# Optimization experiments

Hardware: AMD Instinct MI355X
Metric: run time of the kernel (lower is better)

## Reference

```python
import jax, jax.numpy as jnp
import numpy as np
from jax import lax

B, D, S, H, W, T = 128, 512, 30, 14, 14, 12


def setup_inputs() -> dict:
    key = jax.random.key(0)
    ks = jax.random.split(key, 28)
    f = lambda k, shape: jax.random.normal(k, shape, jnp.float32) * 0.05
    return {
        "q": f(ks[0], (B, D)),
        "cws": f(ks[1], (B, D, S)),
        "KB": f(ks[2], (B, D, H, W)),
        "c0": f(ks[3], (B, D)),
        "m0": f(ks[4], (B, D)),
        "Wq": f(ks[5], (D, D)), "bq": f(ks[6], (D,)),
        "Wct": f(ks[7], (2 * D, D)), "bct": f(ks[8], (D,)),
        "wca": f(ks[9], (D,)), "bca": f(ks[10], ()),
        "Wm": f(ks[11], (D, D)), "bm": f(ks[12], (D,)),
        "Wkb": f(ks[13], (D, D)), "bkb": f(ks[14], (D,)),
        "Wrm": f(ks[15], (2 * D, D)), "brm": f(ks[16], (D,)),
        "wra": f(ks[17], (D,)), "bra": f(ks[18], ()),
        "Wwm": f(ks[19], (2 * D, D)), "bwm": f(ks[20], (D,)),
        "wwa": f(ks[21], (D,)), "bwa": f(ks[22], ()),
        "Wam": f(ks[23], (2 * D, D)), "bam": f(ks[24], (D,)),
        "Wg": f(ks[25], (D, D)), "bg": f(ks[26], (D,)),
        "steps": T,
    }


def _mac(q, cws, KB, c0, m0, Wq, bq, Wct, bct, wca, bca, Wm, bm, Wkb, bkb,
         Wrm, brm, wra, bra, Wwm, bwm, wwa, bwa, Wam, bam, Wg, bg, steps):
    b, d, h, w = KB.shape[0], KB.shape[1], KB.shape[2], KB.shape[3]
    KBp = jnp.transpose(KB, (0, 2, 3, 1))          # B,H,W,d
    KB2 = KBp @ Wkb + bkb                           # KB_transform (step-invariant)
    q_i = q @ Wq + bq                               # q_transform (step-invariant)

    nhist = steps + 1
    c_hist = jnp.zeros((nhist, b, d), KB.dtype).at[0].set(c0)
    m_hist = jnp.zeros((nhist, b, d), KB.dtype).at[0].set(m0)

    def step(carry, t):
        c_hist, m_hist, c_prev, m_prev = carry
        # ---- ControlUnit ----
        cq = jnp.concatenate([q_i, c_prev], axis=-1) @ Wct + bct   # B,d
        clog = jnp.einsum('bds,d->bs', cq[:, :, None] * cws, wca) + bca
        cattn = jax.nn.softmax(clog, axis=-1)                       # B,S
        c_i = jnp.einsum('bs,bds->bd', cattn, cws)
        # ---- ReadUnit ----
        mp = m_prev @ Wm + bm                                       # B,d
        I = mp[:, None, None, :] * KB2                              # B,H,W,d
        Im = jnp.concatenate([I, KBp], axis=-1) @ Wrm + brm         # B,H,W,d
        rlog = jnp.einsum('bhwd,d->bhw', c_i[:, None, None, :] * Im, wra) + bra
        rattn = jax.nn.softmax(rlog.reshape(b, -1), axis=-1).reshape(b, h, w)
        m_new = jnp.einsum('bhw,bhwd->bd', rattn, KBp)
        # ---- WriteUnit (self_attn + mem_gate) ----
        _m = jnp.concatenate([m_new, m_prev], axis=-1) @ Wwm + bwm
        slog = jnp.einsum('tbd,d->bt', c_i[None] * c_hist, wwa) + bwa
        valid = jnp.arange(nhist) <= t
        slog = jnp.where(valid[None, :], slog, jnp.float32(-1e9))
        sattn = jax.nn.softmax(slog, axis=-1)                       # B,T+1
        m_sa = jnp.einsum('bt,tbd->bd', sattn, m_hist)
        _m = jnp.concatenate([m_sa, _m], axis=-1) @ Wam + bam
        g = jax.nn.sigmoid(c_i @ Wg + bg)
        _m = g * m_prev + (1.0 - g) * _m
        c_hist = c_hist.at[t + 1].set(c_i)
        m_hist = m_hist.at[t + 1].set(_m)
        return (c_hist, m_hist, c_i, _m), None

    (c_hist, m_hist, c_last, m_last), _ = lax.scan(
        step, (c_hist, m_hist, c0, m0), jnp.arange(steps))
    return m_last


def reference(q, cws, KB, c0, m0, Wq, bq, Wct, bct, wca, bca, Wm, bm, Wkb, bkb,
              Wrm, brm, wra, bra, Wwm, bwm, wwa, bwa, Wam, bam, Wg, bg, steps):
    return _mac(q, cws, KB, c0, m0, Wq, bq, Wct, bct, wca, bca, Wm, bm, Wkb, bkb,
                Wrm, brm, wra, bra, Wwm, bwm, wwa, bwa, Wam, bam, Wg, bg, steps)
```

## Files before the change

kernel.cpp:

```cpp
#include <hip/hip_runtime.h>
#include <cstdint>

#define BB 128
#define DD 512
#define SS 30
#define PP 196
#define TT 12
#define BD (BB*DD)

typedef unsigned short ushortT;
typedef unsigned int uintT;

__device__ __forceinline__ float bf2f(ushortT u)
{
    return __uint_as_float(((uintT)u) << 16);
}
__device__ __forceinline__ ushortT f2bf(float f)
{
    uintT b = __float_as_uint(f);
    return (ushortT)((b + 0x7FFFu + ((b >> 16) & 1u)) >> 16);
}

struct GDesc {
    const float *A0, *A1;
    const ushortT *W0, *W1;
    const float *bias;
    float *out;
    const float *e1;
    int nparts, epi, mblk, nblk, aux;
};
struct GPack { GDesc d[6]; };

__global__ __launch_bounds__(256)
void gemm4(GPack pk)
{
    GDesc d = pk.d[blockIdx.z];
    if ((int)blockIdx.x >= d.mblk || (int)blockIdx.y >= d.nblk) return;
    const int tid  = threadIdx.x;
    const int lane = tid & 63;
    const int wv   = __builtin_amdgcn_readfirstlane(tid >> 6);

    if (d.epi == 5) {
        int bb = (blockIdx.x * 4 + blockIdx.y) * 2;
        #pragma unroll
        for (int b = bb; b < bb + 2; ++b) {
            const float* sat = d.e1 + b * 16;
            float a0 = 0.f, a1 = 0.f;
            for (int tp = 0; tp <= d.aux; ++tp) {
                float s = sat[tp];
                const float* mh = d.A0 + (size_t)tp * BD + (size_t)b * DD;
                a0 = fmaf(s, mh[tid], a0);
                a1 = fmaf(s, mh[tid + 256], a1);
            }
            d.out[(size_t)b * DD + tid] = a0;
            d.out[(size_t)b * DD + tid + 256] = a1;
        }
        return;
    }

    const int m0 = blockIdx.x * 8;
    const int c0 = blockIdx.y * 128;
    float accx[8], accy[8];
    #pragma unroll
    for (int m = 0; m < 8; ++m) { accx[m] = 0.f; accy[m] = 0.f; }

    for (int p = 0; p < d.nparts; ++p) {
        const float* A = p ? d.A1 : d.A0;
        const ushortT* W = p ? d.W1 : d.W0;
        const float* a = A + (size_t)m0 * 512 + wv * 128;
        const uintT* Wb = (const uintT*)(W + (size_t)(wv * 128) * 512 + c0) + lane;
        #pragma unroll 4
        for (int k = 0; k < 128; ++k) {
            uintT w = Wb[(size_t)k * 256];
            float wx = __uint_as_float(w << 16);
            float wy = __uint_as_float(w & 0xFFFF0000u);
            #pragma unroll
            for (int m = 0; m < 8; ++m) {
                float av = a[m * 512 + k];
                accx[m] = fmaf(av, wx, accx[m]);
                accy[m] = fmaf(av, wy, accy[m]);
            }
        }
    }

    __shared__ float red[4][8][128];
    #pragma unroll
    for (int m = 0; m < 8; ++m)
        *(float2*)&red[wv][m][lane * 2] = make_float2(accx[m], accy[m]);
    __syncthreads();

    for (int i = tid; i < 1024; i += 256) {
        int mm = i >> 7, cl = i & 127;
        float s = (red[0][mm][cl] + red[1][mm][cl])
                + (red[2][mm][cl] + red[3][mm][cl]);
        int row = m0 + mm, col = c0 + cl;
        size_t o = (size_t)row * 512 + col;
        if (d.epi == 0)      d.out[o] = s + d.bias[col];
        else if (d.epi == 1) { float v = s + d.bias[col];
                               d.out[o] = 1.f / (1.f + __expf(-v)); }
        else if (d.epi == 4) d.out[o] = s + d.e1[o];
        else if (d.epi == 7) ((ushortT*)d.out)[o] = f2bf(s);
        else                 d.out[o] = s;
    }
}

struct SP {
    const float *cq, *cws, *wca, *bca, *wra, *wwa, *bwa;
    const ushortT *cwsTh;
    float *c_hist, *sattn, *vb;
    const float *msa, *mnw, *gb, *b2;
    const ushortT *WamH, *WAH, *WBH;
    float *m_hist, *dst;
    int t;
};

__global__ __launch_bounds__(512)
void stepA(SP P)
{
    const int tid = threadIdx.x;
    const int lane = tid & 63;
    __shared__ float cqw[512], ciw[512];
    __shared__ float clog2[32], cattn[32], slog[16];
    __shared__ float red[8][2][128];

    if ((int)blockIdx.x < 128) {
        if (P.t >= TT) return;
        int b = blockIdx.x, w = tid >> 6, t = P.t;
        cqw[tid] = P.cq[(size_t)b*DD + tid] * P.wca[tid];
        __syncthreads();
        for (int s = w; s < SS; s += 8) {
            const ushortT* row = P.cwsTh + ((size_t)b*SS + s)*DD;
            float a = 0.f;
            #pragma unroll
            for (int j = 0; j < 8; ++j)
                a = fmaf(cqw[lane + 64*j], bf2f(row[lane + 64*j]), a);
            for (int off = 32; off; off >>= 1) a += __shfl_xor(a, off, 64);
            if (lane == 0) clog2[s] = a;
        }
        __syncthreads();
        if (tid < 32) {
            float v = (tid < SS) ? clog2[tid] + P.bca[0] : -1e30f;
            float mx = v;
            for (int off = 16; off; off >>= 1) mx = fmaxf(mx, __shfl_xor(mx, off, 32));
            float e = (tid < SS) ? __expf(v - mx) : 0.f;
            float sm = e;
            for (int off = 16; off; off >>= 1) sm += __shfl_xor(sm, off, 32);
            cattn[tid] = e / sm;
        }
        __syncthreads();
        {
            const float* base = P.cws + (size_t)b*DD*SS + (size_t)tid*SS;
            float acc = 0.f;
            #pragma unroll
            for (int j = 0; j < SS; ++j) acc = fmaf(cattn[j], base[j], acc);
            P.c_hist[(size_t)(t+1)*BD + (size_t)b*DD + tid] = acc;
            P.vb[(size_t)b*DD + tid] = acc * P.wra[tid];
            ciw[tid] = acc * P.wwa[tid];
        }
        __syncthreads();
        for (int tp = tid >> 6; tp <= t; tp += 8) {
            const float* ch = P.c_hist + (size_t)tp*BD + (size_t)b*DD;
            float a = 0.f;
            #pragma unroll
            for (int j = 0; j < 8; ++j)
                a = fmaf(ciw[lane + 64*j], ch[lane + 64*j], a);
            for (int off = 32; off; off >>= 1) a += __shfl_xor(a, off, 64);
            if (lane == 0) slog[tp] = a;
        }
        __syncthreads();
        if (tid < 16) {
            float v = (tid <= t) ? slog[tid] + P.bwa[0] : -1e30f;
            float mx = v;
            for (int off = 8; off; off >>= 1) mx = fmaxf(mx, __shfl_xor(mx, off, 16));
            float e = (tid <= t) ? __expf(v - mx) : 0.f;
            float sm = e;
            for (int off = 8; off; off >>= 1) sm += __shfl_xor(sm, off, 16);
            P.sattn[b*16 + tid] = e / sm;
        }
    } else {
        if (P.t == 0) return;
        int gb_ = blockIdx.x - 128;
        int mt = gb_ >> 2, nc = gb_ & 3;
        int wv = __builtin_amdgcn_readfirstlane(tid >> 6);
        const int koff = wv * 64;
        const float* mprev = P.m_hist + (size_t)(P.t - 1) * BD;
        const int r0 = mt * 2;
        float ax0 = 0.f, ay0 = 0.f, ax1 = 0.f, ay1 = 0.f;

        const float* As[3] = { P.msa, P.mnw, mprev };
        const ushortT* Ws[3] = { P.WamH, P.WAH, P.WBH };
        #pragma unroll
        for (int seg = 0; seg < 3; ++seg) {
            const float* a = As[seg] + (size_t)r0 * 512 + koff;
            const uintT* Wb = (const uintT*)(Ws[seg] + (size_t)koff * 512 + nc * 128) + lane;
            #pragma unroll 8
            for (int k = 0; k < 64; ++k) {
                uintT w = Wb[(size_t)k * 256];
                float wx = __uint_as_float(w << 16);
                float wy = __uint_as_float(w & 0xFFFF0000u);
                float av0 = a[k], av1 = a[512 + k];
                ax0 = fmaf(av0, wx, ax0); ay0 = fmaf(av0, wy, ay0);
                ax1 = fmaf(av1, wx, ax1); ay1 = fmaf(av1, wy, ay1);
            }
        }
        *(float2*)&red[wv][0][lane*2] = make_float2(ax0, ay0);
        *(float2*)&red[wv][1][lane*2] = make_float2(ax1, ay1);
        __syncthreads();
        if (tid < 256) {
            int mm = tid >> 7, cl = tid & 127;
            float s = 0.f;
            #pragma unroll
            for (int j = 0; j < 8; ++j) s += red[j][mm][cl];
            int row = r0 + mm, col = nc*128 + cl;
            size_t o = (size_t)row*512 + col;
            float v = s + P.b2[col];
            float g = P.gb[o];
            float pv = mprev[o];
            P.dst[o] = g*pv + (1.f - g)*v;
        }
    }
}

__global__ __launch_bounds__(256)
void read1y(const ushortT* __restrict__ KBh, const float* __restrict__ ubuf,
            const float* __restrict__ mp, const float* __restrict__ WkbT,
            const float* __restrict__ vW, float* __restrict__ rlogp)
{
    int b = blockIdx.x, dg = blockIdx.y, tid = threadIdx.x;
    int lane = tid & 63, w = tid >> 6;
    __shared__ float red[4][64];
    __shared__ float yb[64];
    {
        const float* ur = ubuf + (size_t)b*512;
        const float* mr = mp + (size_t)b*512;
        const float* Wc = WkbT + dg*64 + lane;
        float s = 0.f;
        for (int k = w*128; k < w*128 + 128; ++k)
            s = fmaf(ur[k]*mr[k], Wc[(size_t)k*512], s);
        red[w][lane] = s;
    }
    __syncthreads();
    if (tid < 64)
        yb[tid] = (red[0][tid]+red[1][tid]) + (red[2][tid]+red[3][tid])
                + vW[(size_t)b*512 + dg*64 + tid];
    __syncthreads();
    float a0=0.f, a1=0.f, a2=0.f, a3=0.f;
    if (tid < PP) {
        const ushortT* kb = KBh + ((size_t)b*512 + dg*64)*PP + tid;
        #pragma unroll 4
        for (int dd = 0; dd < 64; dd += 4) {
            a0 = fmaf(bf2f(kb[(size_t)(dd+0)*PP]), yb[dd+0], a0);
            a1 = fmaf(bf2f(kb[(size_t)(dd+1)*PP]), yb[dd+1], a1);
            a2 = fmaf(bf2f(kb[(size_t)(dd+2)*PP]), yb[dd+2], a2);
            a3 = fmaf(bf2f(kb[(size_t)(dd+3)*PP]), yb[dd+3], a3);
        }
    }
    rlogp[((size_t)b*8 + dg)*256 + tid] = (a0+a1)+(a2+a3);
}

__global__ __launch_bounds__(256)
void read2(const ushortT* __restrict__ KBh, const float* __restrict__ rlogp,
           float* __restrict__ m_new)
{
    int b = blockIdx.x, dg = blockIdx.y;
    int tid = threadIdx.x, lane = tid & 63, w = tid >> 6;
    __shared__ float ex[256];
    __shared__ float wred[4];

    float v = -1e30f;
    if (tid < PP) {
        const float* rp = rlogp + (size_t)b*2048 + tid;
        float t0 = rp[0]    + rp[256];
        float t1 = rp[512]  + rp[768];
        float t2 = rp[1024] + rp[1280];
        float t3 = rp[1536] + rp[1792];
        v = (t0+t1)+(t2+t3);
    }
    float mx = v;
    for (int off = 32; off; off >>= 1) mx = fmaxf(mx, __shfl_xor(mx, off, 64));
    if (lane == 0) wred[w] = mx;
    __syncthreads();
    float gmax = fmaxf(fmaxf(wred[0], wred[1]), fmaxf(wred[2], wred[3]));
    float e = (tid < PP) ? __expf(v - gmax) : 0.f;
    float sm = e;
    for (int off = 32; off; off >>= 1) sm += __shfl_xor(sm, off, 64);
    __syncthreads();
    if (lane == 0) wred[w] = sm;
    __syncthreads();
    float inv = 1.f / ((wred[0]+wred[1]) + (wred[2]+wred[3]));
    ex[tid] = e * inv;
    __syncthreads();

    #pragma unroll 2
    for (int i = 0; i < 16; ++i) {
        int d = dg*64 + w*16 + i;
        const ushortT* row = KBh + ((size_t)b*512 + d)*PP;
        float a = ex[lane]       * bf2f(row[lane])
                + ex[lane + 64]  * bf2f(row[lane + 64])
                + ex[lane + 128] * bf2f(row[lane + 128]);
        if (lane < PP - 192) a = fmaf(ex[lane + 192], bf2f(row[lane + 192]), a);
        for (int off = 32; off; off >>= 1) a += __shfl_xor(a, off, 64);
        if (lane == 0) m_new[(size_t)b*512 + d] = a;
    }
}

struct SetupP {
    const float *Wrm, *Wkb, *cws, *KB, *c0v, *m0v, *bwm;
    const float *Wam, *Wam_bot, *bam, *Wg, *Wm, *Wq, *Wct;
    float *WkbT, *c_hist, *m_hist, *b2;
    ushortT *KBh, *cwsTh, *WamH, *WgH, *WmH, *WqH, *WambH, *WctHt, *WctHb;
    ushortT *WrmTuH, *WrmTvH;
};

__global__ __launch_bounds__(256)
void setup_misc(SetupP P)
{
    __shared__ float tile[32][33];
    int id = blockIdx.x, tid = threadIdx.x;

    if (id < 768) {
        int which = id >> 8, tj = id & 255;
        const float* src = (which == 0) ? P.Wrm
                         : (which == 1) ? (P.Wrm + 512*512) : P.Wkb;
        int bx = (tj & 15) * 32, by = (tj >> 4) * 32;
        int tx = tid & 31, ty = tid >> 5;
        #pragma unroll
        for (int i = 0; i < 32; i += 8)
            tile[ty+i][tx] = src[(size_t)(by+ty+i)*512 + bx+tx];
        __syncthreads();
        if (which == 2) {
            #pragma unroll
            for (int i = 0; i < 32; i += 8)
                P.WkbT[(size_t)(bx+ty+i)*512 + by+tx] = tile[tx][ty+i];
        } else {
            ushortT* dst = which ? P.WrmTvH : P.WrmTuH;
            #pragma unroll
            for (int i = 0; i < 32; i += 8)
                dst[(size_t)(bx+ty+i)*512 + by+tx] = f2bf(tile[tx][ty+i]);
        }
    } else if (id < 2816) {
        int j = id - 768;
        int b = j >> 4, dc = j & 15;
        const float* src = P.cws + ((size_t)b*DD + dc*32) * SS;
        for (int i = tid; i < 1024; i += 256) {
            int r = i >> 5, s = i & 31;
            if (s < SS) tile[r][s] = src[(size_t)r*SS + s];
        }
        __syncthreads();
        for (int i = tid; i < 1024; i += 256) {
            int s = i >> 5, r = i & 31;
            if (s < SS)
                P.cwsTh[((size_t)b*SS + s)*DD + dc*32 + r] = f2bf(tile[r][s]);
        }
    } else if (id < 9088) {
        size_t i = ((size_t)(id - 2816) * 256 + tid) * 8;
        #pragma unroll
        for (int j = 0; j < 8; ++j)
            P.KBh[i + j] = f2bf(P.KB[i + j]);
    } else if (id < 9344) {
        int i = (id - 9088) * 256 + tid;
        P.c_hist[i] = P.c0v[i];
        P.m_hist[i] = P.m0v[i];
    } else if (id < 9352) {
        int lane = tid & 63, w = tid >> 6;
        int n = (id - 9344) * 64 + lane;
        float s = 0.f;
        for (int k = w*128; k < w*128 + 128; ++k)
            s = fmaf(P.bwm[k], P.Wam_bot[(size_t)k*512 + n], s);
        __shared__ float red[4][64];
        red[w][lane] = s;
        __syncthreads();
        if (tid < 64) {
            int nn = (id - 9344) * 64 + tid;
            P.b2[nn] = red[0][tid] + red[1][tid] + red[2][tid] + red[3][tid]
                     + P.bam[nn];
        }
    } else {
        int j = id - 9352;
        int which = j >> 7, blk = j & 127;
        const float* src = (which == 0) ? P.Wam
                         : (which == 1) ? P.Wg
                         : (which == 2) ? P.Wm
                         : (which == 3) ? P.Wq
                         : (which == 4) ? P.Wam_bot
                         : (which == 5) ? P.Wct : (P.Wct + 512*512);
        ushortT* dst = (which == 0) ? P.WamH
                     : (which == 1) ? P.WgH
                     : (which == 2) ? P.WmH
                     : (which == 3) ? P.WqH
                     : (which == 4) ? P.WambH
                     : (which == 5) ? P.WctHt : P.WctHb;
        size_t i = ((size_t)blk * 256 + tid) * 8;
        #pragma unroll
        for (int jj = 0; jj < 8; ++jj)
            dst[i + jj] = f2bf(src[i + jj]);
    }
}

extern "C" void kernel_launch(void* const* d_in, const int* in_sizes, int n_in,
                              void* d_out, int out_size, void* d_ws, size_t ws_size,
                              hipStream_t stream)
{
    (void)in_sizes; (void)n_in; (void)out_size; (void)ws_size;
    const float* q   = (const float*)d_in[0];
    const float* cws = (const float*)d_in[1];
    const float* KB  = (const float*)d_in[2];
    const float* c0  = (const float*)d_in[3];
    const float* m0  = (const float*)d_in[4];
    const float* Wq  = (const float*)d_in[5];
    const float* bq  = (const float*)d_in[6];
    const float* Wct = (const float*)d_in[7];
    const float* bct = (const float*)d_in[8];
    const float* wca = (const float*)d_in[9];
    const float* bca = (const float*)d_in[10];
    const float* Wm  = (const float*)d_in[11];
    const float* bm  = (const float*)d_in[12];
    const float* Wkb = (const float*)d_in[13];
    const float* Wrm = (const float*)d_in[15];
    const float* wra = (const float*)d_in[17];
    const float* Wwm = (const float*)d_in[19];
    const float* bwm = (const float*)d_in[20];
    const float* wwa = (const float*)d_in[21];
    const float* bwa = (const float*)d_in[22];
    const float* Wam = (const float*)d_in[23];
    const float* bam = (const float*)d_in[24];
    const float* Wg  = (const float*)d_in[25];
    const float* bg  = (const float*)d_in[26];

    float* ws      = (float*)d_ws;
    float* c_hist  = ws;
    float* m_hist  = ws + 13*BD;
    float* qct     = ws + 26*BD;
    float* q_i     = ws + 27*BD;
    float* cq      = ws + 28*BD;
    float* mp      = ws + 29*BD;
    float* vb      = ws + 30*BD;
    float* ubuf    = ws + 31*BD;
    float* vW      = ws + 32*BD;
    float* gb      = ws + 33*BD;
    float* msa     = ws + 34*BD;
    float* mnw     = ws + 35*BD;
    float* sattn   = ws + 36*BD;
    float* rlogp   = ws + 37*BD;
    float* WkbT    = ws + 49*BD;
    float* b2      = ws + 61*BD;
    ushortT* cwsTh = (ushortT*)(ws + 62*BD);
    ushortT* KBh   = (ushortT*)(ws + 92*BD);
    ushortT* WamH  = (ushortT*)(ws + 190*BD);
    ushortT* WAH   = (ushortT*)(ws + 192*BD);
    ushortT* WBH   = (ushortT*)(ws + 194*BD);
    ushortT* WgH   = (ushortT*)(ws + 196*BD);
    ushortT* WmH   = (ushortT*)(ws + 198*BD);
    ushortT* WqH   = (ushortT*)(ws + 200*BD);
    ushortT* WambH = (ushortT*)(ws + 202*BD);
    ushortT* WctHt = (ushortT*)(ws + 204*BD);
    ushortT* WctHb = (ushortT*)(ws + 206*BD);
    ushortT* WrmTuH= (ushortT*)(ws + 208*BD);
    ushortT* WrmTvH= (ushortT*)(ws + 210*BD);

    const float* Wam_bot = Wam + 512*512;
    const float* Wwm_bot = Wwm + 512*512;
    dim3 blk(256);
    GDesc Z = { nullptr,nullptr,nullptr,nullptr,nullptr,nullptr,nullptr,
                1, 6, 0, 0, 0 };

    {
        SetupP S;
        S.Wrm = Wrm; S.Wkb = Wkb; S.cws = cws; S.KB = KB;
        S.c0v = c0; S.m0v = m0; S.bwm = bwm;
        S.Wam = Wam; S.Wam_bot = Wam_bot; S.bam = bam;
        S.Wg = Wg; S.Wm = Wm; S.Wq = Wq; S.Wct = Wct;
        S.WkbT = WkbT; S.c_hist = c_hist; S.m_hist = m_hist; S.b2 = b2;
        S.KBh = KBh; S.cwsTh = cwsTh;
        S.WamH = WamH; S.WgH = WgH; S.WmH = WmH; S.WqH = WqH;
        S.WambH = WambH; S.WctHt = WctHt; S.WctHb = WctHb;
        S.WrmTuH = WrmTuH; S.WrmTvH = WrmTvH;
        setup_misc<<<dim3(10248), blk, 0, stream>>>(S);
    }
    {
        GPack pk;
        pk.d[0] = { Wwm, nullptr, WambH, nullptr, nullptr, (float*)WAH,
                    nullptr, 1, 7, 64, 4, 0 };
        pk.d[1] = { Wwm_bot, nullptr, WambH, nullptr, nullptr, (float*)WBH,
                    nullptr, 1, 7, 64, 4, 0 };
        pk.d[2] = { q, nullptr, WqH, nullptr, bq, q_i, nullptr,
                    1, 0, 16, 4, 0 };
        pk.d[3] = Z; pk.d[4] = Z; pk.d[5] = Z;
        gemm4<<<dim3(64,4,3), blk, 0, stream>>>(pk);
    }
    {
        GPack pk;
        pk.d[0] = { q_i, nullptr, WctHt, nullptr, bct, qct, nullptr,
                    1, 0, 16, 4, 0 };
        pk.d[1] = { q_i, c0, WctHt, WctHb, bct, cq, nullptr,
                    2, 0, 16, 4, 0 };
        pk.d[2] = Z; pk.d[3] = Z; pk.d[4] = Z; pk.d[5] = Z;
        gemm4<<<dim3(16,4,2), blk, 0, stream>>>(pk);
    }

    for (int t = 0; t <= TT; ++t) {
        {
            SP P;
            P.cq = cq; P.cws = cws; P.cwsTh = cwsTh;
            P.wca = wca; P.bca = bca; P.wra = wra; P.wwa = wwa; P.bwa = bwa;
            P.c_hist = c_hist; P.sattn = sattn; P.vb = vb;
            P.msa = msa; P.mnw = mnw; P.gb = gb; P.b2 = b2;
            P.WamH = WamH; P.WAH = WAH; P.WBH = WBH;
            P.m_hist = m_hist;
            P.dst = (t == TT) ? (float*)d_out : (m_hist + (size_t)t * BD);
            P.t = t;
            stepA<<<dim3(384), dim3(512), 0, stream>>>(P);
        }
        if (t == TT) break;

        float* c_i = c_hist + (size_t)(t+1) * BD;
        {
            GPack pk;
            pk.d[0] = { vb, nullptr, WrmTuH, nullptr, nullptr, ubuf, nullptr,
                        1, 6, 16, 4, 0 };
            pk.d[1] = { vb, nullptr, WrmTvH, nullptr, nullptr, vW, nullptr,
                        1, 6, 16, 4, 0 };
            pk.d[2] = { c_i, nullptr, WgH, nullptr, bg, gb, nullptr,
                        1, 1, 16, 4, 0 };
            pk.d[3] = { c_i, nullptr, WctHb, nullptr, nullptr, cq, qct,
                        1, 4, 16, 4, 0 };
            pk.d[4] = { m_hist + (size_t)t * BD, nullptr, WmH, nullptr, bm, mp,
                        nullptr, 1, 0, 16, 4, 0 };
            pk.d[5] = { m_hist, nullptr, nullptr, nullptr, nullptr, msa, sattn,
                        1, 5, 16, 4, t };
            gemm4<<<dim3(16,4,6), blk, 0, stream>>>(pk);
        }
        read1y<<<dim3(BB,8), blk, 0, stream>>>(KBh, ubuf, mp, WkbT, vW, rlogp);
        read2<<<dim3(BB,8), blk, 0, stream>>>(KBh, rlogp, mnw);
    }
}
```

Before: 756.3 us.

## Read cws and Wkb transpose as bf16, vectorize setup bf16 conversions

stepA's context-weighted sum now reads the bf16 transposed copy cwsTh (coalesced across threads) instead of strided fp32 cws, and read1y reads a bf16 transposed Wkb instead of fp32. The setup kernel writes WkbT as bf16 and converts KB and weights with float4 loads and packed uint4 stores. The aim is to halve memory traffic in the per-step kernels and fix uncoalesced access, at some precision cost in c_i and the y projection.

```diff
diff --git a/kernel.cpp b/kernel.cpp
--- a/kernel.cpp
+++ b/kernel.cpp
@@ -19,6 +19,10 @@
 {
     uintT b = __float_as_uint(f);
     return (ushortT)((b + 0x7FFFu + ((b >> 16) & 1u)) >> 16);
+}
+__device__ __forceinline__ uintT pack2bf(float lo, float hi)
+{
+    return (uintT)f2bf(lo) | ((uintT)f2bf(hi) << 16);
 }
 
 struct GDesc {
@@ -105,7 +109,7 @@
 }
 
 struct SP {
-    const float *cq, *cws, *wca, *bca, *wra, *wwa, *bwa;
+    const float *cq, *wca, *bca, *wra, *wwa, *bwa;
     const ushortT *cwsTh;
     float *c_hist, *sattn, *vb;
     const float *msa, *mnw, *gb, *b2;
@@ -149,10 +153,11 @@
         }
         __syncthreads();
         {
-            const float* base = P.cws + (size_t)b*DD*SS + (size_t)tid*SS;
+            const ushortT* baseh = P.cwsTh + (size_t)b*SS*DD + tid;
             float acc = 0.f;
             #pragma unroll
-            for (int j = 0; j < SS; ++j) acc = fmaf(cattn[j], base[j], acc);
+            for (int j = 0; j < SS; ++j)
+                acc = fmaf(cattn[j], bf2f(baseh[(size_t)j*DD]), acc);
             P.c_hist[(size_t)(t+1)*BD + (size_t)b*DD + tid] = acc;
             P.vb[(size_t)b*DD + tid] = acc * P.wra[tid];
             ciw[tid] = acc * P.wwa[tid];
@@ -223,7 +228,7 @@
 
 __global__ __launch_bounds__(256)
 void read1y(const ushortT* __restrict__ KBh, const float* __restrict__ ubuf,
-            const float* __restrict__ mp, const float* __restrict__ WkbT,
+            const float* __restrict__ mp, const ushortT* __restrict__ WkbTh,
             const float* __restrict__ vW, float* __restrict__ rlogp)
 {
     int b = blockIdx.x, dg = blockIdx.y, tid = threadIdx.x;
@@ -233,10 +238,10 @@
     {
         const float* ur = ubuf + (size_t)b*512;
         const float* mr = mp + (size_t)b*512;
-        const float* Wc = WkbT + dg*64 + lane;
+        const ushortT* Wc = WkbTh + dg*64 + lane;
         float s = 0.f;
         for (int k = w*128; k < w*128 + 128; ++k)
-            s = fmaf(ur[k]*mr[k], Wc[(size_t)k*512], s);
+            s = fmaf(ur[k]*mr[k], bf2f(Wc[(size_t)k*512]), s);
         red[w][lane] = s;
     }
     __syncthreads();
@@ -307,9 +312,9 @@
 struct SetupP {
     const float *Wrm, *Wkb, *cws, *KB, *c0v, *m0v, *bwm;
     const float *Wam, *Wam_bot, *bam, *Wg, *Wm, *Wq, *Wct;
-    float *WkbT, *c_hist, *m_hist, *b2;
+    float *c_hist, *m_hist, *b2;
     ushortT *KBh, *cwsTh, *WamH, *WgH, *WmH, *WqH, *WambH, *WctHt, *WctHb;
-    ushortT *WrmTuH, *WrmTvH;
+    ushortT *WrmTuH, *WrmTvH, *WkbTH;
 };
 
 __global__ __launch_bounds__(256)
@@ -322,22 +327,17 @@
         int which = id >> 8, tj = id & 255;
         const float* src = (which == 0) ? P.Wrm
                          : (which == 1) ? (P.Wrm + 512*512) : P.Wkb;
+        ushortT* dst = (which == 0) ? P.WrmTuH
+                     : (which == 1) ? P.WrmTvH : P.WkbTH;
         int bx = (tj & 15) * 32, by = (tj >> 4) * 32;
         int tx = tid & 31, ty = tid >> 5;
         #pragma unroll
         for (int i = 0; i < 32; i += 8)
             tile[ty+i][tx] = src[(size_t)(by+ty+i)*512 + bx+tx];
         __syncthreads();
-        if (which == 2) {
-            #pragma unroll
-            for (int i = 0; i < 32; i += 8)
-                P.WkbT[(size_t)(bx+ty+i)*512 + by+tx] = tile[tx][ty+i];
-        } else {
-            ushortT* dst = which ? P.WrmTvH : P.WrmTuH;
-            #pragma unroll
-            for (int i = 0; i < 32; i += 8)
-                dst[(size_t)(bx+ty+i)*512 + by+tx] = f2bf(tile[tx][ty+i]);
-        }
+        #pragma unroll
+        for (int i = 0; i < 32; i += 8)
+            dst[(size_t)(bx+ty+i)*512 + by+tx] = f2bf(tile[tx][ty+i]);
     } else if (id < 2816) {
         int j = id - 768;
         int b = j >> 4, dc = j & 15;
@@ -354,9 +354,14 @@
         }
     } else if (id < 9088) {
         size_t i = ((size_t)(id - 2816) * 256 + tid) * 8;
-        #pragma unroll
-        for (int j = 0; j < 8; ++j)
-            P.KBh[i + j] = f2bf(P.KB[i + j]);
+        const float4* s4 = (const float4*)(P.KB + i);
+        float4 v0 = s4[0], v1 = s4[1];
+        uint4 o;
+        o.x = pack2bf(v0.x, v0.y);
+        o.y = pack2bf(v0.z, v0.w);
+        o.z = pack2bf(v1.x, v1.y);
+        o.w = pack2bf(v1.z, v1.w);
+        *(uint4*)(P.KBh + i) = o;
     } else if (id < 9344) {
         int i = (id - 9088) * 256 + tid;
         P.c_hist[i] = P.c0v[i];
@@ -391,9 +396,14 @@
                      : (which == 4) ? P.WambH
                      : (which == 5) ? P.WctHt : P.WctHb;
         size_t i = ((size_t)blk * 256 + tid) * 8;
-        #pragma unroll
-        for (int jj = 0; jj < 8; ++jj)
-            dst[i + jj] = f2bf(src[i + jj]);
+        const float4* s4 = (const float4*)(src + i);
+        float4 v0 = s4[0], v1 = s4[1];
+        uint4 o;
+        o.x = pack2bf(v0.x, v0.y);
+        o.y = pack2bf(v0.z, v0.w);
+        o.z = pack2bf(v1.x, v1.y);
+        o.w = pack2bf(v1.z, v1.w);
+        *(uint4*)(dst + i) = o;
     }
 }
 
@@ -442,7 +452,7 @@
     float* mnw     = ws + 35*BD;
     float* sattn   = ws + 36*BD;
     float* rlogp   = ws + 37*BD;
-    float* WkbT    = ws + 49*BD;
+    ushortT* WkbTH = (ushortT*)(ws + 49*BD);
     float* b2      = ws + 61*BD;
     ushortT* cwsTh = (ushortT*)(ws + 62*BD);
     ushortT* KBh   = (ushortT*)(ws + 92*BD);
@@ -470,11 +480,11 @@
         S.c0v = c0; S.m0v = m0; S.bwm = bwm;
         S.Wam = Wam; S.Wam_bot = Wam_bot; S.bam = bam;
         S.Wg = Wg; S.Wm = Wm; S.Wq = Wq; S.Wct = Wct;
-        S.WkbT = WkbT; S.c_hist = c_hist; S.m_hist = m_hist; S.b2 = b2;
+        S.c_hist = c_hist; S.m_hist = m_hist; S.b2 = b2;
         S.KBh = KBh; S.cwsTh = cwsTh;
         S.WamH = WamH; S.WgH = WgH; S.WmH = WmH; S.WqH = WqH;
         S.WambH = WambH; S.WctHt = WctHt; S.WctHb = WctHb;
-        S.WrmTuH = WrmTuH; S.WrmTvH = WrmTvH;
+        S.WrmTuH = WrmTuH; S.WrmTvH = WrmTvH; S.WkbTH = WkbTH;
         setup_misc<<<dim3(10248), blk, 0, stream>>>(S);
     }
     {
@@ -501,7 +511,7 @@
     for (int t = 0; t <= TT; ++t) {
         {
             SP P;
-            P.cq = cq; P.cws = cws; P.cwsTh = cwsTh;
+            P.cq = cq; P.cwsTh = cwsTh;
             P.wca = wca; P.bca = bca; P.wra = wra; P.wwa = wwa; P.bwa = bwa;
             P.c_hist = c_hist; P.sattn = sattn; P.vb = vb;
             P.msa = msa; P.mnw = mnw; P.gb = gb; P.b2 = b2;
@@ -530,7 +540,7 @@
                         1, 5, 16, 4, t };
             gemm4<<<dim3(16,4,6), blk, 0, stream>>>(pk);
         }
-        read1y<<<dim3(BB,8), blk, 0, stream>>>(KBh, ubuf, mp, WkbT, vW, rlogp);
+        read1y<<<dim3(BB,8), blk, 0, stream>>>(KBh, ubuf, mp, WkbTH, vW, rlogp);
         read2<<<dim3(BB,8), blk, 0, stream>>>(KBh, rlogp, mnw);
     }
 }
```

New measurement: 747.8 us (median of 4 runs). No clear change (-1.1%).
